# Kernel tuning notes

Measured on AMD Instinct MI355X. Metric: run time of the kernel, lower is better.

Reference implementation:

```python
import jax, jax.numpy as jnp
import numpy as np

IN_CH, IN_U, OUT_CH, OUT_U = 1152, 8, 10, 16
BATCH = 256
ROUTING_EPOCH = 3


def squash(s, axis=-1):
    # v = (||s||^2 / (1 + ||s||^2)) * s / ||s||
    sqn = jnp.sum(s * s, axis=axis, keepdims=True)
    return s * (sqn / ((1.0 + sqn) * jnp.sqrt(sqn + 1e-9)))


def setup_inputs() -> dict:
    key = jax.random.key(0)
    k1, k2 = jax.random.split(key)
    inp = jax.random.normal(k1, (BATCH, IN_CH, IN_U), dtype=jnp.float32)
    W = jax.random.normal(k2, (IN_CH, OUT_CH, OUT_U, IN_U), dtype=jnp.float32)
    return {"inp": inp, "W": W}


def reference(inp, W):
    # u_hat[b,i,o,u] = sum_k W[i,o,u,k] * inp[b,i,k]   -> [B, 1152, 10, 16]
    u_hat = jnp.einsum('iouk,bik->biou', W, inp)
    B = inp.shape[0]
    b = jnp.zeros((IN_CH, OUT_CH), dtype=inp.dtype)  # routing logits [1152, 10]
    v = None
    for _ in range(ROUTING_EPOCH):
        c = jax.nn.softmax(b, axis=1)                 # [1152, 10]
        s = jnp.einsum('biou,io->bou', u_hat, c)      # sum over input capsules -> [B, 10, 16]
        v = squash(s, axis=-1)                        # [B, 10, 16]
        # delta_b[i,o] = mean_b sum_u u_hat[b,i,o,u] * v[b,o,u]
        b = b + jnp.einsum('biou,bou->io', u_hat, v) / B
    return v  # == original v.squeeze(): [B, 10, 16]
```

## Files before the change

### kernel.cpp

```cpp
#include <hip/hip_runtime.h>
#include <math.h>

#define NB 256
#define IC 1152
#define OC 10
#define OU 16
#define IK 8
#define KTOT (IC * IK)
#define NTOT (OC * OU)
#define S_KS 16

typedef __attribute__((ext_vector_type(8))) short short8;
typedef __attribute__((ext_vector_type(4))) float f32x4;

static __device__ __forceinline__ unsigned short f2bf(float f) {
    unsigned u = __float_as_uint(f);
    unsigned r = (u + 0x7FFF + ((u >> 16) & 1)) >> 16;
    return (unsigned short)r;
}

__global__ __launch_bounds__(256) void prep_kernel(
    const float* __restrict__ inp,
    float* __restrict__ blog,
    unsigned short* __restrict__ inpb,
    unsigned short* __restrict__ inpT)
{
    const int kt  = blockIdx.x;
    const int bt  = blockIdx.y;
    const int tid = threadIdx.x;

    {
        int bid = blockIdx.y * 144 + blockIdx.x;
        if (bid < 45) blog[bid * 256 + tid] = 0.f;
    }

    __shared__ unsigned short sh[64][65];

#pragma unroll
    for (int j = 0; j < 4; ++j) {
        int q     = j * 256 + tid;
        int b_loc = q >> 4;
        int kq    = (q & 15) * 4;
        float4 g = *(const float4*)&inp[(size_t)(bt * 64 + b_loc) * KTOT + kt * 64 + kq];
        unsigned short h0 = f2bf(g.x), h1 = f2bf(g.y), h2 = f2bf(g.z), h3 = f2bf(g.w);
        sh[kq][b_loc] = h0; sh[kq + 1][b_loc] = h1;
        sh[kq + 2][b_loc] = h2; sh[kq + 3][b_loc] = h3;
        short4 pk = { (short)h0, (short)h1, (short)h2, (short)h3 };
        *(short4*)&inpb[(size_t)(bt * 64 + b_loc) * KTOT + kt * 64 + kq] = pk;
    }
    __syncthreads();

#pragma unroll
    for (int j = 0; j < 4; ++j) {
        int q     = j * 256 + tid;
        int k_loc = q >> 4;
        int b4    = (q & 15) * 4;
        short4 pk = { (short)sh[k_loc][b4],     (short)sh[k_loc][b4 + 1],
                      (short)sh[k_loc][b4 + 2], (short)sh[k_loc][b4 + 3] };
        *(short4*)&inpT[(size_t)(kt * 64 + k_loc) * 256 + bt * 64 + b4] = pk;
    }
}

#define BLP 584
__global__ __launch_bounds__(256) void spass_kernel(
    const unsigned short* __restrict__ inpb,
    const float* __restrict__ W,
    const float* __restrict__ blog,
    float* __restrict__ part)
{
    const int bid  = blockIdx.x;
    const int nt   = bid % 10;
    const int ks   = (bid / 10) % 16;
    const int mtg  = bid / 160;
    const int tid  = threadIdx.x;
    const int w    = tid >> 6;
    const int lane = tid & 63;
    const int l15  = lane & 15;
    const int koff = (lane >> 4) * 8;
    const int k0   = ks * 576;
    const int i0   = ks * 72;
    const int mt   = mtg * 4 + w;

    __shared__ unsigned short Bl[16 * BLP];
    __shared__ float c_loc[72];

    if (tid < 72) {
        const float* br = &blog[(size_t)(i0 + tid) * OC];
        float x[OC], m = -1e30f;
#pragma unroll
        for (int o = 0; o < OC; ++o) { x[o] = br[o]; m = fmaxf(m, x[o]); }
        float ssum = 0.f;
#pragma unroll
        for (int o = 0; o < OC; ++o) ssum += expf(x[o] - m);
        c_loc[tid] = expf(x[nt] - m) / ssum;
    }
    __syncthreads();

#pragma unroll
    for (int jj = 0; jj < 5; ++jj) {
        int q = jj * 256 + tid;
        if (q < 1152) {
            int i_loc = q >> 4, u = q & 15;
            const float* wr = W + (((size_t)(i0 + i_loc) * OC + nt) * OU + u) * IK;
            float4 a = *(const float4*)wr;
            float4 b = *(const float4*)(wr + 4);
            float cc = c_loc[i_loc];
            union { short8 v; unsigned short us[8]; } pk;
            pk.us[0] = f2bf(cc * a.x); pk.us[1] = f2bf(cc * a.y);
            pk.us[2] = f2bf(cc * a.z); pk.us[3] = f2bf(cc * a.w);
            pk.us[4] = f2bf(cc * b.x); pk.us[5] = f2bf(cc * b.y);
            pk.us[6] = f2bf(cc * b.z); pk.us[7] = f2bf(cc * b.w);
            *(short8*)&Bl[u * BLP + i_loc * 8] = pk.v;
        }
    }
    __syncthreads();

    const unsigned short* ap  = inpb + (size_t)(mt * 16 + l15) * KTOT + k0 + koff;
    const unsigned short* bls = &Bl[l15 * BLP + koff];

    f32x4 acc = {0.f, 0.f, 0.f, 0.f};
#pragma unroll
    for (int kk = 0; kk < 18; ++kk) {
        short8 av = *(const short8*)(ap + kk * 32);
        short8 bv = *(const short8*)(bls + kk * 32);
        acc = __builtin_amdgcn_mfma_f32_16x16x32_bf16(av, bv, acc, 0, 0, 0);
    }

    float* pp = part + ((size_t)ks * NB + mt * 16 + (lane >> 4) * 4) * NTOT + nt * 16 + l15;
#pragma unroll
    for (int r = 0; r < 4; ++r)
        pp[(size_t)r * NTOT] = acc[r];
}

__global__ __launch_bounds__(256) void reduce_squash_kernel(
    const float* __restrict__ part, float* __restrict__ vout,
    unsigned short* __restrict__ vT)
{
    const int tid = threadIdx.x;
    const int el  = tid & 31;
    const int kl  = tid >> 5;
    const int e   = blockIdx.x * 32 + el;

    float a = part[(size_t)(kl * 2) * (NB * NTOT) + e]
            + part[(size_t)(kl * 2 + 1) * (NB * NTOT) + e];

    __shared__ float red[8][36];
    red[kl][el] = a;
    __syncthreads();

    if (tid < 32) {
        float s = ((red[0][el] + red[1][el]) + (red[2][el] + red[3][el]))
                + ((red[4][el] + red[5][el]) + (red[6][el] + red[7][el]));
        float sq = s * s;
        sq += __shfl_xor(sq, 1);
        sq += __shfl_xor(sq, 2);
        sq += __shfl_xor(sq, 4);
        sq += __shfl_xor(sq, 8);
        float vv = s * (sq / ((1.f + sq) * sqrtf(sq + 1e-9f)));
        vout[e] = vv;
        int n = e % NTOT, b = e / NTOT;
        vT[(size_t)n * 256 + b] = f2bf(vv);
    }
}

__global__ __launch_bounds__(256) void delta_kernel(
    const unsigned short* __restrict__ inpT,
    const unsigned short* __restrict__ vT,
    const float* __restrict__ W,
    float* __restrict__ blog)
{
    const int g    = blockIdx.x * 4 + (threadIdx.x >> 6);
    const int lane = threadIdx.x & 63;
    const int mt   = g % 576;
    const int ntp  = g / 576;
    const int l15  = lane & 15;
    const int quad = lane >> 4;
    const int koff = quad * 8;
    const int nt0  = ntp * 2;

    const unsigned short* ap  = inpT + (size_t)(mt * 16 + l15) * 256 + koff;
    const unsigned short* bp0 = vT   + (size_t)(nt0 * 16 + l15) * 256 + koff;
    const unsigned short* bp1 = bp0 + 16 * 256;

    f32x4 acc0 = {0.f, 0.f, 0.f, 0.f};
    f32x4 acc1 = {0.f, 0.f, 0.f, 0.f};
#pragma unroll
    for (int kk = 0; kk < 8; ++kk) {
        short8 av = *(const short8*)(ap  + kk * 32);
        short8 b0 = *(const short8*)(bp0 + kk * 32);
        short8 b1 = *(const short8*)(bp1 + kk * 32);
        acc0 = __builtin_amdgcn_mfma_f32_16x16x32_bf16(av, b0, acc0, 0, 0, 0);
        acc1 = __builtin_amdgcn_mfma_f32_16x16x32_bf16(av, b1, acc1, 0, 0, 0);
    }

    const int i = mt * 2 + (quad >> 1);
    const float* wr0 = W + (((size_t)i * OC + nt0) * OU + l15) * IK + (quad & 1) * 4;
    float4 wf0 = *(const float4*)wr0;
    float4 wf1 = *(const float4*)(wr0 + OU * IK);
    float w0 = wf0.x * acc0[0] + wf0.y * acc0[1] + wf0.z * acc0[2] + wf0.w * acc0[3];
    float w1 = wf1.x * acc1[0] + wf1.y * acc1[1] + wf1.z * acc1[2] + wf1.w * acc1[3];

#pragma unroll
    for (int d = 0; d < 5; ++d) {
        int m = (d == 0) ? 16 : (1 << (d - 1));
        w0 += __shfl_xor(w0, m);
        w1 += __shfl_xor(w1, m);
    }

    if ((lane & 31) == 0) {
        blog[(size_t)i * OC + nt0]     += w0 * (1.0f / NB);
        blog[(size_t)i * OC + nt0 + 1] += w1 * (1.0f / NB);
    }
}

extern "C" void kernel_launch(void* const* d_in, const int* in_sizes, int n_in,
                              void* d_out, int out_size, void* d_ws, size_t ws_size,
                              hipStream_t stream) {
    const float* inp = (const float*)d_in[0];
    const float* W   = (const float*)d_in[1];
    float* vout = (float*)d_out;

    float* blog = (float*)d_ws;
    float* part = blog + IC * OC;
    unsigned short* inpb = (unsigned short*)(part + (size_t)S_KS * NB * NTOT);
    unsigned short* inpT = inpb + (size_t)NB * KTOT;
    unsigned short* vT   = inpT + (size_t)KTOT * 256;

    prep_kernel<<<dim3(144, 4), dim3(256), 0, stream>>>(inp, blog, inpb, inpT);

    for (int t = 0; t < 3; ++t) {
        spass_kernel<<<dim3(640), dim3(256), 0, stream>>>(inpb, W, blog, part);
        reduce_squash_kernel<<<dim3(NB * NTOT / 32), dim3(256), 0, stream>>>(part, vout, vT);
        if (t < 2)
            delta_kernel<<<dim3(720), dim3(256), 0, stream>>>(inpT, vT, W, blog);
    }
}
```

Before: 128.5 us.

## Fuse first routing pass into prep kernel using uniform coupling, simplify reduce

The prep kernel now also runs the first s-pass. Extra blocks compute the first-iteration partial sums straight from fp32 inputs, converting to bf16 on the fly. Because the logits start at zero, the softmax is replaced by the constant 1/OC, so the prep and first routing pass share a launch and the first softmax is skipped. The reduce-squash kernel is rewritten so each thread sums all 16 K-split partials directly without shared memory, using fewer blocks. This removes one launch and a dependency stage, at the cost of each fused block converting its A tile redundantly from fp32.

```diff
diff --git a/kernel.cpp b/kernel.cpp
--- a/kernel.cpp
+++ b/kernel.cpp
@@ -9,6 +9,7 @@
 #define KTOT (IC * IK)
 #define NTOT (OC * OU)
 #define S_KS 16
+#define BLP 584
 
 typedef __attribute__((ext_vector_type(8))) short short8;
 typedef __attribute__((ext_vector_type(4))) float f32x4;
@@ -19,49 +20,103 @@
     return (unsigned short)r;
 }
 
-__global__ __launch_bounds__(256) void prep_kernel(
+__global__ __launch_bounds__(256) void k1_spass0_prep(
     const float* __restrict__ inp,
+    const float* __restrict__ W,
     float* __restrict__ blog,
+    float* __restrict__ part,
     unsigned short* __restrict__ inpb,
     unsigned short* __restrict__ inpT)
 {
-    const int kt  = blockIdx.x;
-    const int bt  = blockIdx.y;
+    const int blk = blockIdx.x;
     const int tid = threadIdx.x;
 
-    {
-        int bid = blockIdx.y * 144 + blockIdx.x;
-        if (bid < 45) blog[bid * 256 + tid] = 0.f;
-    }
-
-    __shared__ unsigned short sh[64][65];
-
-#pragma unroll
-    for (int j = 0; j < 4; ++j) {
-        int q     = j * 256 + tid;
-        int b_loc = q >> 4;
-        int kq    = (q & 15) * 4;
-        float4 g = *(const float4*)&inp[(size_t)(bt * 64 + b_loc) * KTOT + kt * 64 + kq];
-        unsigned short h0 = f2bf(g.x), h1 = f2bf(g.y), h2 = f2bf(g.z), h3 = f2bf(g.w);
-        sh[kq][b_loc] = h0; sh[kq + 1][b_loc] = h1;
-        sh[kq + 2][b_loc] = h2; sh[kq + 3][b_loc] = h3;
-        short4 pk = { (short)h0, (short)h1, (short)h2, (short)h3 };
-        *(short4*)&inpb[(size_t)(bt * 64 + b_loc) * KTOT + kt * 64 + kq] = pk;
-    }
-    __syncthreads();
-
-#pragma unroll
-    for (int j = 0; j < 4; ++j) {
-        int q     = j * 256 + tid;
-        int k_loc = q >> 4;
-        int b4    = (q & 15) * 4;
-        short4 pk = { (short)sh[k_loc][b4],     (short)sh[k_loc][b4 + 1],
-                      (short)sh[k_loc][b4 + 2], (short)sh[k_loc][b4 + 3] };
-        *(short4*)&inpT[(size_t)(kt * 64 + k_loc) * 256 + bt * 64 + b4] = pk;
-    }
-}
-
-#define BLP 584
+    __shared__ unsigned short Bl[16 * BLP];
+
+    if (blk < 640) {
+        const int nt   = blk % 10;
+        const int ks   = (blk / 10) % 16;
+        const int mtg  = blk / 160;
+        const int w    = tid >> 6;
+        const int lane = tid & 63;
+        const int l15  = lane & 15;
+        const int koff = (lane >> 4) * 8;
+        const int k0   = ks * 576;
+        const int i0   = ks * 72;
+        const int mt   = mtg * 4 + w;
+
+#pragma unroll
+        for (int jj = 0; jj < 5; ++jj) {
+            int q = jj * 256 + tid;
+            if (q < 1152) {
+                int i_loc = q >> 4, u = q & 15;
+                const float* wr = W + (((size_t)(i0 + i_loc) * OC + nt) * OU + u) * IK;
+                float4 a = *(const float4*)wr;
+                float4 b = *(const float4*)(wr + 4);
+                const float cc = 0.1f;
+                union { short8 v; unsigned short us[8]; } pk;
+                pk.us[0] = f2bf(cc * a.x); pk.us[1] = f2bf(cc * a.y);
+                pk.us[2] = f2bf(cc * a.z); pk.us[3] = f2bf(cc * a.w);
+                pk.us[4] = f2bf(cc * b.x); pk.us[5] = f2bf(cc * b.y);
+                pk.us[6] = f2bf(cc * b.z); pk.us[7] = f2bf(cc * b.w);
+                *(short8*)&Bl[u * BLP + i_loc * 8] = pk.v;
+            }
+        }
+        __syncthreads();
+
+        const float* af = inp + (size_t)(mt * 16 + l15) * KTOT + k0 + koff;
+        const unsigned short* bls = &Bl[l15 * BLP + koff];
+
+        f32x4 acc = {0.f, 0.f, 0.f, 0.f};
+#pragma unroll
+        for (int kk = 0; kk < 18; ++kk) {
+            float4 a0 = *(const float4*)(af + kk * 32);
+            float4 a1 = *(const float4*)(af + kk * 32 + 4);
+            union { short8 v; unsigned short us[8]; } A;
+            A.us[0] = f2bf(a0.x); A.us[1] = f2bf(a0.y);
+            A.us[2] = f2bf(a0.z); A.us[3] = f2bf(a0.w);
+            A.us[4] = f2bf(a1.x); A.us[5] = f2bf(a1.y);
+            A.us[6] = f2bf(a1.z); A.us[7] = f2bf(a1.w);
+            short8 bv = *(const short8*)(bls + kk * 32);
+            acc = __builtin_amdgcn_mfma_f32_16x16x32_bf16(A.v, bv, acc, 0, 0, 0);
+        }
+
+        float* pp = part + ((size_t)ks * NB + mt * 16 + (lane >> 4) * 4) * NTOT + nt * 16 + l15;
+#pragma unroll
+        for (int r = 0; r < 4; ++r)
+            pp[(size_t)r * NTOT] = acc[r];
+    } else {
+        const int vb = blk - 640;
+        const int kt = vb % 144;
+        const int bt = vb / 144;
+        if (vb < 45) blog[vb * 256 + tid] = 0.f;
+
+        auto sh = (unsigned short (*)[65])Bl;
+#pragma unroll
+        for (int j = 0; j < 4; ++j) {
+            int q     = j * 256 + tid;
+            int b_loc = q >> 4;
+            int kq    = (q & 15) * 4;
+            float4 g = *(const float4*)&inp[(size_t)(bt * 64 + b_loc) * KTOT + kt * 64 + kq];
+            unsigned short h0 = f2bf(g.x), h1 = f2bf(g.y), h2 = f2bf(g.z), h3 = f2bf(g.w);
+            sh[kq][b_loc] = h0; sh[kq + 1][b_loc] = h1;
+            sh[kq + 2][b_loc] = h2; sh[kq + 3][b_loc] = h3;
+            short4 pk = { (short)h0, (short)h1, (short)h2, (short)h3 };
+            *(short4*)&inpb[(size_t)(bt * 64 + b_loc) * KTOT + kt * 64 + kq] = pk;
+        }
+        __syncthreads();
+#pragma unroll
+        for (int j = 0; j < 4; ++j) {
+            int q     = j * 256 + tid;
+            int k_loc = q >> 4;
+            int b4    = (q & 15) * 4;
+            short4 pk = { (short)sh[k_loc][b4],     (short)sh[k_loc][b4 + 1],
+                          (short)sh[k_loc][b4 + 2], (short)sh[k_loc][b4 + 3] };
+            *(short4*)&inpT[(size_t)(kt * 64 + k_loc) * 256 + bt * 64 + b4] = pk;
+        }
+    }
+}
+
 __global__ __launch_bounds__(256) void spass_kernel(
     const unsigned short* __restrict__ inpb,
     const float* __restrict__ W,
@@ -95,7 +150,6 @@
         c_loc[tid] = expf(x[nt] - m) / ssum;
     }
     __syncthreads();
-
 #pragma unroll
     for (int jj = 0; jj < 5; ++jj) {
         int q = jj * 256 + tid;
@@ -117,7 +171,6 @@
 
     const unsigned short* ap  = inpb + (size_t)(mt * 16 + l15) * KTOT + k0 + koff;
     const unsigned short* bls = &Bl[l15 * BLP + koff];
-
     f32x4 acc = {0.f, 0.f, 0.f, 0.f};
 #pragma unroll
     for (int kk = 0; kk < 18; ++kk) {
@@ -125,7 +178,6 @@
         short8 bv = *(const short8*)(bls + kk * 32);
         acc = __builtin_amdgcn_mfma_f32_16x16x32_bf16(av, bv, acc, 0, 0, 0);
     }
-
     float* pp = part + ((size_t)ks * NB + mt * 16 + (lane >> 4) * 4) * NTOT + nt * 16 + l15;
 #pragma unroll
     for (int r = 0; r < 4; ++r)
@@ -136,31 +188,20 @@
     const float* __restrict__ part, float* __restrict__ vout,
     unsigned short* __restrict__ vT)
 {
-    const int tid = threadIdx.x;
-    const int el  = tid & 31;
-    const int kl  = tid >> 5;
-    const int e   = blockIdx.x * 32 + el;
-
-    float a = part[(size_t)(kl * 2) * (NB * NTOT) + e]
-            + part[(size_t)(kl * 2 + 1) * (NB * NTOT) + e];
-
-    __shared__ float red[8][36];
-    red[kl][el] = a;
-    __syncthreads();
-
-    if (tid < 32) {
-        float s = ((red[0][el] + red[1][el]) + (red[2][el] + red[3][el]))
-                + ((red[4][el] + red[5][el]) + (red[6][el] + red[7][el]));
-        float sq = s * s;
-        sq += __shfl_xor(sq, 1);
-        sq += __shfl_xor(sq, 2);
-        sq += __shfl_xor(sq, 4);
-        sq += __shfl_xor(sq, 8);
-        float vv = s * (sq / ((1.f + sq) * sqrtf(sq + 1e-9f)));
-        vout[e] = vv;
-        int n = e % NTOT, b = e / NTOT;
-        vT[(size_t)n * 256 + b] = f2bf(vv);
-    }
+    const int gtid = blockIdx.x * 256 + threadIdx.x;
+    float s = 0.f;
+#pragma unroll
+    for (int ks = 0; ks < 16; ++ks)
+        s += part[(size_t)ks * (NB * NTOT) + gtid];
+    float sq = s * s;
+    sq += __shfl_xor(sq, 1);
+    sq += __shfl_xor(sq, 2);
+    sq += __shfl_xor(sq, 4);
+    sq += __shfl_xor(sq, 8);
+    float vv = s * (sq / ((1.f + sq) * sqrtf(sq + 1e-9f)));
+    vout[gtid] = vv;
+    int n = gtid % NTOT, b = gtid / NTOT;
+    vT[(size_t)n * 256 + b] = f2bf(vv);
 }
 
 __global__ __launch_bounds__(256) void delta_kernel(
@@ -192,21 +233,18 @@
         acc0 = __builtin_amdgcn_mfma_f32_16x16x32_bf16(av, b0, acc0, 0, 0, 0);
         acc1 = __builtin_amdgcn_mfma_f32_16x16x32_bf16(av, b1, acc1, 0, 0, 0);
     }
-
     const int i = mt * 2 + (quad >> 1);
     const float* wr0 = W + (((size_t)i * OC + nt0) * OU + l15) * IK + (quad & 1) * 4;
     float4 wf0 = *(const float4*)wr0;
     float4 wf1 = *(const float4*)(wr0 + OU * IK);
     float w0 = wf0.x * acc0[0] + wf0.y * acc0[1] + wf0.z * acc0[2] + wf0.w * acc0[3];
     float w1 = wf1.x * acc1[0] + wf1.y * acc1[1] + wf1.z * acc1[2] + wf1.w * acc1[3];
-
 #pragma unroll
     for (int d = 0; d < 5; ++d) {
         int m = (d == 0) ? 16 : (1 << (d - 1));
         w0 += __shfl_xor(w0, m);
         w1 += __shfl_xor(w1, m);
     }
-
     if ((lane & 31) == 0) {
         blog[(size_t)i * OC + nt0]     += w0 * (1.0f / NB);
         blog[(size_t)i * OC + nt0 + 1] += w1 * (1.0f / NB);
@@ -226,12 +264,12 @@
     unsigned short* inpT = inpb + (size_t)NB * KTOT;
     unsigned short* vT   = inpT + (size_t)KTOT * 256;
 
-    prep_kernel<<<dim3(144, 4), dim3(256), 0, stream>>>(inp, blog, inpb, inpT);
-
-    for (int t = 0; t < 3; ++t) {
-        spass_kernel<<<dim3(640), dim3(256), 0, stream>>>(inpb, W, blog, part);
-        reduce_squash_kernel<<<dim3(NB * NTOT / 32), dim3(256), 0, stream>>>(part, vout, vT);
-        if (t < 2)
-            delta_kernel<<<dim3(720), dim3(256), 0, stream>>>(inpT, vT, W, blog);
-    }
-}
+    k1_spass0_prep<<<dim3(1216), dim3(256), 0, stream>>>(inp, W, blog, part, inpb, inpT);
+    reduce_squash_kernel<<<dim3(160), dim3(256), 0, stream>>>(part, vout, vT);
+    delta_kernel<<<dim3(720), dim3(256), 0, stream>>>(inpT, vT, W, blog);
+    spass_kernel<<<dim3(640), dim3(256), 0, stream>>>(inpb, W, blog, part);
+    reduce_squash_kernel<<<dim3(160), dim3(256), 0, stream>>>(part, vout, vT);
+    delta_kernel<<<dim3(720), dim3(256), 0, stream>>>(inpT, vT, W, blog);
+    spass_kernel<<<dim3(640), dim3(256), 0, stream>>>(inpb, W, blog, part);
+    reduce_squash_kernel<<<dim3(160), dim3(256), 0, stream>>>(part, vout, vT);
+}
```

After: 130.1 us. No clear change (+1.2%).
